# Performance work log

Hardware: AMD Instinct MI355X
Metric: run time of the kernel (lower is better)

Reference implementation:

```python
import jax, jax.numpy as jnp
import numpy as np

NUM_HEADS = 8
KEY_DIM = 512  # d_gain = 1/sqrt(key_dim) in the original (NOT per-head dim)
MASK_FILL = -1000000.0


def setup_inputs() -> dict:
    key = jax.random.key(0)
    ks = jax.random.split(key, 6)
    N, Tq, Tk, D, U = 8, 1024, 1024, 512, 512
    query = jax.random.normal(ks[0], (N, Tq, D), dtype=jnp.float32)
    key_t = jax.random.normal(ks[1], (N, Tk, D), dtype=jnp.float32)
    key_mask = jax.random.randint(ks[2], (N, Tk), 0, 2).astype(bool)
    Wq = jax.random.normal(ks[3], (D, U), dtype=jnp.float32) / np.sqrt(D)
    Wk = jax.random.normal(ks[4], (D, U), dtype=jnp.float32) / np.sqrt(D)
    Wv = jax.random.normal(ks[5], (D, U), dtype=jnp.float32) / np.sqrt(D)
    return {"query": query, "key": key_t, "key_mask": key_mask,
            "Wq": Wq, "Wk": Wk, "Wv": Wv}


def reference(query, key, key_mask, Wq, Wk, Wv):
    N, Tq, _ = query.shape
    Tk = key.shape[1]
    U = Wq.shape[1]
    h = NUM_HEADS
    d = U // h
    scale = 1.0 / (KEY_DIM ** 0.5)

    # projections then split heads: [N,T,U] -> [h,N,T,d]
    q = (query @ Wq).reshape(N, Tq, h, d).transpose(2, 0, 1, 3)
    k = (key @ Wk).reshape(N, Tk, h, d).transpose(2, 0, 1, 3)
    v = (key @ Wv).reshape(N, Tk, h, d).transpose(2, 0, 1, 3)

    scores = scale * jnp.einsum('hnqd,hnkd->hnqk', q, k)
    scores = jnp.where(key_mask[None, :, None, :], scores, MASK_FILL)
    attn = jax.nn.softmax(scores, axis=3)
    out = jnp.einsum('hnqk,hnkd->hnqd', attn, v)
    # merge heads: [h,N,Tq,d] -> [N,Tq,h*d]
    return out.transpose(1, 2, 0, 3).reshape(N, Tq, U)
```

## Files before the change

kernel.cpp:

```cpp
#include <hip/hip_runtime.h>
#include <hip/hip_bf16.h>

typedef unsigned short u16;
typedef __attribute__((ext_vector_type(8))) short short8;
typedef __attribute__((ext_vector_type(4))) short short4v;
typedef __attribute__((ext_vector_type(4))) float f32x4;

#define NB 8
#define TT 1024
#define DD 512
#define UU 512
#define HH 8
#define DH 64
#define SCALE 0.044194173824159216f
#define LOG2E 1.4426950408889634f
#define MASK_FILL_2 -1442695.0f

__device__ __forceinline__ float ld_flex(const void* p, long i, bool f32) {
  if (f32) return ((const float*)p)[i];
  unsigned int u = (unsigned int)(((const u16*)p)[i]) << 16;
  return __uint_as_float(u);
}

__device__ __forceinline__ u16 f32_to_bf16(float f) {
  unsigned int u = __float_as_uint(f);
  unsigned int r = (u + 0x7FFFu + ((u >> 16) & 1u)) >> 16;
  return (u16)r;
}

__device__ __forceinline__ float ex2(float x) {
#if __has_builtin(__builtin_amdgcn_exp2f)
  return __builtin_amdgcn_exp2f(x);
#else
  return __expf(x * 0.6931471805599453f);
#endif
}

__device__ __forceinline__ unsigned int pk_bf16(float a, float b) {
  union { __hip_bfloat162 h2; unsigned int u; } c;
  c.h2 = __float22bfloat162_rn(make_float2(a, b));
  return c.u;
}

__device__ __forceinline__ void gld16(const void* g, void* l) {
  __builtin_amdgcn_global_load_lds(
      (const __attribute__((address_space(1))) unsigned int*)g,
      (__attribute__((address_space(3))) unsigned int*)l, 16, 0, 0);
}

#define CONV_BLOCKS 2048
#define WT_BLOCKS 768
#define MASK_BLOCKS 32

__global__ __launch_bounds__(256) void prep_kernel(
    const void* __restrict__ query, const void* __restrict__ key,
    const void* __restrict__ W0, const void* __restrict__ W1,
    const void* __restrict__ W2, const void* __restrict__ mask,
    u16* __restrict__ Xq, u16* __restrict__ Xk, u16* __restrict__ Wt,
    float* __restrict__ maskadd, int* __restrict__ flags) {
  __shared__ float tile[32][33];
  __shared__ int s_f32, s_mi32;
  const int b = blockIdx.x, tid = threadIdx.x;

  if (tid == 0) { s_f32 = 0; s_mi32 = 1; }
  __syncthreads();
  {
    const u16* qh = (const u16*)query;
    int weird = 0;
#pragma unroll
    for (int p = 0; p < 4; ++p) {
      unsigned int u = (unsigned int)qh[tid * 4 + p] << 16;
      float v = __uint_as_float(u);
      if (!(v == v) || fabsf(v) > 1e6f) weird = 1;
    }
    if (weird) atomicOr(&s_f32, 1);
    const unsigned int* mi = (const unsigned int*)mask;
    if (mi[tid * 2] > 1u || mi[tid * 2 + 1] > 1u) atomicAnd(&s_mi32, 0);
  }
  __syncthreads();
  const bool f32 = s_f32 != 0;
  const bool mi32 = s_mi32 != 0;
  if (b == CONV_BLOCKS && tid == 0) { flags[0] = s_f32; flags[1] = s_mi32; }

  if (b < CONV_BLOCKS) {
    if (!f32) return;
#pragma unroll
    for (int p = 0; p < 4; ++p) {
      const int i = b * 256 + tid + p * (CONV_BLOCKS * 256);
      const void* in = (i < 1048576) ? query : key;
      u16* outp = (i < 1048576) ? Xq : Xk;
      const int j = i & 1048575;
      float4 v = ((const float4*)in)[j];
      ushort4 o;
      o.x = f32_to_bf16(v.x); o.y = f32_to_bf16(v.y);
      o.z = f32_to_bf16(v.z); o.w = f32_to_bf16(v.w);
      ((ushort4*)outp)[j] = o;
    }
  } else if (b < CONV_BLOCKS + WT_BLOCKS) {
    const int lb = b - CONV_BLOCKS;
    const int z = lb >> 8, rem = lb & 255;
    const int k0 = (rem & 15) * 32, n0 = (rem >> 4) * 32;
    const void* W = (z == 0) ? W0 : (z == 1) ? W1 : W2;
    const float sc = (z == 0) ? SCALE * LOG2E : 1.0f;
    u16* out = Wt + (size_t)z * DD * UU;
#pragma unroll
    for (int p = 0; p < 4; ++p) {
      int i = (tid >> 5) + p * 8, j = tid & 31;
      tile[i][j] = ld_flex(W, (long)(k0 + i) * UU + n0 + j, f32);
    }
    __syncthreads();
#pragma unroll
    for (int p = 0; p < 4; ++p) {
      int nl = (tid >> 5) + p * 8, kl = tid & 31;
      out[(size_t)(n0 + nl) * DD + k0 + kl] = f32_to_bf16(tile[kl][nl] * sc);
    }
  } else {
    const int i = (b - CONV_BLOCKS - WT_BLOCKS) * 256 + tid;
    bool mv = mi32 ? (((const int*)mask)[i] != 0)
                   : (((const unsigned char*)mask)[i] != 0);
    maskadd[i] = mv ? 0.0f : MASK_FILL_2;
  }
}

__global__ __launch_bounds__(256) void proj_mfma(
    const void* __restrict__ query, const void* __restrict__ key,
    const u16* __restrict__ Xq, const u16* __restrict__ Xk,
    const u16* __restrict__ Wt, u16* __restrict__ Qp, u16* __restrict__ Kp,
    u16* __restrict__ Vt, const int* __restrict__ flags) {
  __shared__ __align__(16) u16 smem[128 * 136];
  const bool f32 = flags[0] != 0;
  const int lid = blockIdx.x + (blockIdx.y << 6) + (blockIdx.z << 8);
  const int swz = (lid & 7) * 96 + (lid >> 3);
  const int bx = swz & 63, by = (swz >> 6) & 3, z = swz >> 8;
  const u16* X = (z == 0) ? (f32 ? Xq : (const u16*)query)
                          : (f32 ? Xk : (const u16*)key);
  const u16* Wz = Wt + (size_t)z * DD * UU;
  const int m0 = bx * 128, n0 = by * 128;
  const int tid = threadIdx.x;
  const int w = tid >> 6, l = tid & 63;
  const int quad = l >> 4, l15 = l & 15;
  const int wm = (w >> 1) * 64, wn = (w & 1) * 64;

  const int c0 = w * 128 + l;
  const int row0 = c0 >> 2, q0 = (c0 & 3) * 8;
  const int c1 = c0 + 64;
  const int row1 = c1 >> 2, q1 = (c1 & 3) * 8;
  const u16* aS0 = X + (size_t)(m0 + row0) * DD + q0;
  const u16* aS1 = X + (size_t)(m0 + row1) * DD + q1;
  const u16* bS0 = Wz + (size_t)(n0 + row0) * DD + q0;
  const u16* bS1 = Wz + (size_t)(n0 + row1) * DD + q1;
  const int dD0 = w * 1024;
  const int dD1 = w * 1024 + 512;

  f32x4 acc[4][4];
#pragma unroll
  for (int mi = 0; mi < 4; ++mi)
#pragma unroll
    for (int ni = 0; ni < 4; ++ni)
#pragma unroll
      for (int r = 0; r < 4; ++r) acc[mi][ni][r] = 0.0f;

  gld16(aS0, smem + dD0);
  gld16(aS1, smem + dD1);
  gld16(bS0, smem + 4096 + dD0);
  gld16(bS1, smem + 4096 + dD1);

#pragma unroll 1
  for (int t = 0; t < 16; ++t) {
    const int co = (t & 1) * 8192;
    if (t < 15) {
      const int k1 = (t + 1) * 32;
      const int no = ((t + 1) & 1) * 8192;
      gld16(aS0 + k1, smem + no + dD0);
      gld16(aS1 + k1, smem + no + dD1);
      gld16(bS0 + k1, smem + no + 4096 + dD0);
      gld16(bS1 + k1, smem + no + 4096 + dD1);
      asm volatile("s_waitcnt vmcnt(4)" ::: "memory");
    } else {
      asm volatile("s_waitcnt vmcnt(0)" ::: "memory");
    }
    __builtin_amdgcn_s_barrier();

    short8 af[4], bf[4];
#pragma unroll
    for (int mi = 0; mi < 4; ++mi)
      af[mi] = *(const short8*)&smem[co + (wm + mi * 16 + l15) * 32 + quad * 8];
#pragma unroll
    for (int ni = 0; ni < 4; ++ni)
      bf[ni] = *(const short8*)&smem[co + 4096 + (wn + ni * 16 + l15) * 32 + quad * 8];
#pragma unroll
    for (int mi = 0; mi < 4; ++mi)
#pragma unroll
      for (int ni = 0; ni < 4; ++ni)
        acc[mi][ni] = __builtin_amdgcn_mfma_f32_16x16x32_bf16(
            af[mi], bf[ni], acc[mi][ni], 0, 0, 0);
    __builtin_amdgcn_s_barrier();
  }

  if (z < 2) {
#pragma unroll
    for (int mi = 0; mi < 4; ++mi)
#pragma unroll
      for (int ni = 0; ni < 4; ++ni) {
        const int ml = wm + mi * 16 + quad * 4;
        const int nl = wn + ni * 16 + l15;
#pragma unroll
        for (int r = 0; r < 4; ++r)
          smem[(ml + r) * 136 + nl] = f32_to_bf16(acc[mi][ni][r]);
      }
  } else {
#pragma unroll
    for (int mi = 0; mi < 4; ++mi)
#pragma unroll
      for (int ni = 0; ni < 4; ++ni) {
        const int ml = wm + mi * 16 + quad * 4;
        const int nl = wn + ni * 16 + l15;
        ushort4 pk;
        pk.x = f32_to_bf16(acc[mi][ni][0]);
        pk.y = f32_to_bf16(acc[mi][ni][1]);
        pk.z = f32_to_bf16(acc[mi][ni][2]);
        pk.w = f32_to_bf16(acc[mi][ni][3]);
        *(ushort4*)&smem[nl * 136 + ml] = pk;
      }
  }
  __syncthreads();

  if (z < 2) {
    u16* outp = (z == 0) ? Qp : Kp;
#pragma unroll
    for (int p = 0; p < 8; ++p) {
      const int idx = tid + p * 256;
      const int row = idx >> 4, c8 = (idx & 15) * 8;
      short8 v = *(const short8*)&smem[row * 136 + c8];
      *(short8*)&outp[(size_t)(m0 + row) * UU + n0 + c8] = v;
    }
  } else {
    const int nb = m0 >> 10, tk0 = m0 & 1023;
#pragma unroll
    for (int p = 0; p < 8; ++p) {
      const int idx = tid + p * 256;
      const int row = idx >> 4, c8 = (idx & 15) * 8;
      const int u = n0 + row, h = u >> 6, dh = u & 63;
      short8 v = *(const short8*)&smem[row * 136 + c8];
      *(short8*)&Vt[(size_t)((nb * HH + h) * DH + dh) * TT + tk0 + c8] = v;
    }
  }
}

__global__ __launch_bounds__(256, 4) void attn_mfma(
    const u16* __restrict__ Qp, const u16* __restrict__ Kp,
    const u16* __restrict__ Vt, const float* __restrict__ maskadd,
    void* __restrict__ out, const int* __restrict__ flags) {
  __shared__ __align__(16) char smem[35072];
  u16* sU = (u16*)smem;
  const int tid = threadIdx.x;
  const int w = tid >> 6, l = tid & 63;
  const int quad = l >> 4, l15 = l & 15;
  const int lid = blockIdx.x + (blockIdx.y << 4) + (blockIdx.z << 7);
  const int swz = (lid & 7) * 128 + (lid >> 3);
  const int qt = swz & 15, h = (swz >> 4) & 7, n = swz >> 7;
  const int q0 = qt * 64;
  const bool f32o = flags[0] != 0;
  u16* s_mask = sU + 16384;
  float* lp = (float*)(smem + 34816);

  {
    float4 m4 = ((const float4*)(maskadd + n * TT))[tid];
    ushort4 mu;
    mu.x = f32_to_bf16(m4.x); mu.y = f32_to_bf16(m4.y);
    mu.z = f32_to_bf16(m4.z); mu.w = f32_to_bf16(m4.w);
    ((ushort4*)s_mask)[tid] = mu;
  }

  const u16* qbase = Qp + (size_t)(n * TT + q0 + w * 16 + l15) * UU + h * DH + quad * 8;
  short8 bq[2];
  bq[0] = *(const short8*)(qbase);
  bq[1] = *(const short8*)(qbase + 32);

  const int lr = l >> 3, ls = l & 7;
  const u16* kc = Kp + (size_t)(n * TT + w * 16 + lr) * UU + h * DH + ((ls ^ lr) * 8);
  const u16* vc = Vt + (size_t)((n * HH + h) * DH + w * 16 + lr) * TT + ((ls ^ lr) * 8);

  const int srcA = ((quad & 1) << 5) + l15;
  const int srcB = srcA + 16;
  const bool hiK = (quad >> 1) != 0;

  f32x4 o[4];
  float lsum = 0.0f;
#pragma unroll
  for (int ni = 0; ni < 4; ++ni)
#pragma unroll
    for (int r = 0; r < 4; ++r) o[ni][r] = 0.0f;

  __syncthreads();

  gld16(kc, smem + w * 2048);
  gld16(kc + 8 * UU, smem + w * 2048 + 1024);
  gld16(vc, smem + 16384 + w * 2048);
  gld16(vc + 8 * TT, smem + 16384 + w * 2048 + 1024);

#pragma unroll 1
  for (int t = 0; t < 16; ++t) {
    const int co = (t & 1) * 4096;
    if (t < 15) {
      const int no = ((t + 1) & 1) * 8192;
      const u16* kn = kc + (size_t)(t + 1) * 64 * UU;
      const u16* vn = vc + (t + 1) * 64;
      gld16(kn, smem + no + w * 2048);
      gld16(kn + 8 * UU, smem + no + w * 2048 + 1024);
      gld16(vn, smem + 16384 + no + w * 2048);
      gld16(vn + 8 * TT, smem + 16384 + no + w * 2048 + 1024);
      asm volatile("s_waitcnt vmcnt(4)" ::: "memory");
    } else {
      asm volatile("s_waitcnt vmcnt(0)" ::: "memory");
    }
    __builtin_amdgcn_s_barrier();

#pragma unroll
    for (int ss = 0; ss < 2; ++ss) {
      short8 ak[2][2];
#pragma unroll
      for (int ktl = 0; ktl < 2; ++ktl)
#pragma unroll
        for (int kd = 0; kd < 2; ++kd)
          ak[ktl][kd] = *(const short8*)&sU[co + (ss * 32 + ktl * 16 + l15) * 64 +
                                            (((kd * 4 + quad) ^ (l15 & 7)) * 8)];

      f32x4 s[2];
      __builtin_amdgcn_s_setprio(1);
#pragma unroll
      for (int ktl = 0; ktl < 2; ++ktl) {
#pragma unroll
        for (int r = 0; r < 4; ++r) s[ktl][r] = 0.0f;
#pragma unroll
        for (int kd = 0; kd < 2; ++kd)
          s[ktl] = __builtin_amdgcn_mfma_f32_16x16x32_bf16(
              ak[ktl][kd], bq[kd], s[ktl], 0, 0, 0);
      }
      __builtin_amdgcn_s_setprio(0);

      const int kb = t * 64 + ss * 32;
      unsigned int u00, u01, u10, u11;
      {
        ushort4 m0u = *(const ushort4*)&s_mask[kb + quad * 4];
        ushort4 m1u = *(const ushort4*)&s_mask[kb + 16 + quad * 4];
        float e0 = ex2(s[0][0] + __uint_as_float((unsigned)m0u.x << 16));
        float e1 = ex2(s[0][1] + __uint_as_float((unsigned)m0u.y << 16));
        float e2 = ex2(s[0][2] + __uint_as_float((unsigned)m0u.z << 16));
        float e3 = ex2(s[0][3] + __uint_as_float((unsigned)m0u.w << 16));
        float f0 = ex2(s[1][0] + __uint_as_float((unsigned)m1u.x << 16));
        float f1 = ex2(s[1][1] + __uint_as_float((unsigned)m1u.y << 16));
        float f2 = ex2(s[1][2] + __uint_as_float((unsigned)m1u.z << 16));
        float f3 = ex2(s[1][3] + __uint_as_float((unsigned)m1u.w << 16));
        lsum += ((e0 + e1) + (e2 + e3)) + ((f0 + f1) + (f2 + f3));
        u00 = pk_bf16(e0, e1); u01 = pk_bf16(e2, e3);
        u10 = pk_bf16(f0, f1); u11 = pk_bf16(f2, f3);
      }

      short8 ap;
      {
        unsigned int a0k0 = __shfl(u00, srcA), a0k1 = __shfl(u10, srcA);
        unsigned int a1k0 = __shfl(u01, srcA), a1k1 = __shfl(u11, srcA);
        unsigned int a2k0 = __shfl(u00, srcB), a2k1 = __shfl(u10, srcB);
        unsigned int a3k0 = __shfl(u01, srcB), a3k1 = __shfl(u11, srcB);
        union { unsigned int d[4]; short8 v; } pu;
        pu.d[0] = hiK ? a0k1 : a0k0;
        pu.d[1] = hiK ? a1k1 : a1k0;
        pu.d[2] = hiK ? a2k1 : a2k0;
        pu.d[3] = hiK ? a3k1 : a3k0;
        ap = pu.v;
      }

      short8 vf[4];
#pragma unroll
      for (int ni = 0; ni < 4; ++ni)
        vf[ni] = *(const short8*)&sU[8192 + co + (ni * 16 + l15) * 64 +
                                     (((ss * 4 + quad) ^ (l15 & 7)) * 8)];

      __builtin_amdgcn_s_setprio(1);
#pragma unroll
      for (int ni = 0; ni < 4; ++ni)
        o[ni] = __builtin_amdgcn_mfma_f32_16x16x32_bf16(ap, vf[ni], o[ni], 0, 0, 0);
      __builtin_amdgcn_s_setprio(0);
    }

    __builtin_amdgcn_s_barrier();
  }

  lsum += __shfl_xor(lsum, 16);
  lsum += __shfl_xor(lsum, 32);
  if (l < 16) lp[w * 16 + l] = lsum;
  __syncthreads();

  float den[4];
#pragma unroll
  for (int r = 0; r < 4; ++r) den[r] = lp[w * 16 + quad * 4 + r];

#pragma unroll
  for (int ni = 0; ni < 4; ++ni)
#pragma unroll
    for (int r = 0; r < 4; ++r) {
      const int q = q0 + w * 16 + quad * 4 + r;
      const float v = o[ni][r] / den[r];
      const size_t idx = (size_t)(n * TT + q) * UU + h * DH + ni * 16 + l15;
      if (f32o) ((float*)out)[idx] = v;
      else ((u16*)out)[idx] = f32_to_bf16(v);
    }
}

extern "C" void kernel_launch(void* const* d_in, const int* in_sizes, int n_in,
                              void* d_out, int out_size, void* d_ws, size_t ws_size,
                              hipStream_t stream) {
  const void* query = d_in[0];
  const void* key   = d_in[1];
  const void* mask  = d_in[2];
  const void* Wq    = d_in[3];
  const void* Wk    = d_in[4];
  const void* Wv    = d_in[5];

  char* base = (char*)d_ws;
  int* flags = (int*)base;
  float* maskadd = (float*)(base + 256);
  u16* Wt  = (u16*)(base + 64 * 1024);
  u16* Xq  = Wt + (size_t)3 * DD * UU;
  u16* Xk  = Xq + (size_t)NB * TT * DD;
  u16* Qp  = Xk + (size_t)NB * TT * DD;
  u16* Kp  = Qp + (size_t)NB * TT * UU;
  u16* Vtp = Kp + (size_t)NB * TT * UU;

  prep_kernel<<<CONV_BLOCKS + WT_BLOCKS + MASK_BLOCKS, 256, 0, stream>>>(
      query, key, Wq, Wk, Wv, mask, Xq, Xk, Wt, maskadd, flags);

  dim3 pgrid(NB * TT / 128, UU / 128, 3);
  proj_mfma<<<pgrid, 256, 0, stream>>>(query, key, Xq, Xk, Wt, Qp, Kp, Vtp, flags);

  dim3 agrid(TT / 64, HH, NB);
  attn_mfma<<<agrid, 256, 0, stream>>>(Qp, Kp, Vtp, maskadd, d_out, flags);
}
```

Baseline: 152.5 us.

## Split attention key range across two wave groups with shared-memory reduction

```diff
diff --git a/kernel.cpp b/kernel.cpp
--- a/kernel.cpp
+++ b/kernel.cpp
@@ -247,15 +247,16 @@
   }
 }
 
-__global__ __launch_bounds__(256, 4) void attn_mfma(
+__global__ __launch_bounds__(512, 8) void attn_mfma(
     const u16* __restrict__ Qp, const u16* __restrict__ Kp,
     const u16* __restrict__ Vt, const float* __restrict__ maskadd,
     void* __restrict__ out, const int* __restrict__ flags) {
-  __shared__ __align__(16) char smem[35072];
+  __shared__ __align__(16) char smem[35328];
   u16* sU = (u16*)smem;
   const int tid = threadIdx.x;
   const int w = tid >> 6, l = tid & 63;
   const int quad = l >> 4, l15 = l & 15;
+  const int qsub = w & 3, ks = w >> 2;
   const int lid = blockIdx.x + (blockIdx.y << 4) + (blockIdx.z << 7);
   const int swz = (lid & 7) * 128 + (lid >> 3);
   const int qt = swz & 15, h = (swz >> 4) & 7, n = swz >> 7;
@@ -264,7 +265,7 @@
   u16* s_mask = sU + 16384;
   float* lp = (float*)(smem + 34816);
 
-  {
+  if (tid < 256) {
     float4 m4 = ((const float4*)(maskadd + n * TT))[tid];
     ushort4 mu;
     mu.x = f32_to_bf16(m4.x); mu.y = f32_to_bf16(m4.y);
@@ -272,14 +273,19 @@
     ((ushort4*)s_mask)[tid] = mu;
   }
 
-  const u16* qbase = Qp + (size_t)(n * TT + q0 + w * 16 + l15) * UU + h * DH + quad * 8;
+  const u16* qbase = Qp + (size_t)(n * TT + q0 + qsub * 16 + l15) * UU + h * DH + quad * 8;
   short8 bq[2];
   bq[0] = *(const short8*)(qbase);
   bq[1] = *(const short8*)(qbase + 32);
 
-  const int lr = l >> 3, ls = l & 7;
-  const u16* kc = Kp + (size_t)(n * TT + w * 16 + lr) * UU + h * DH + ((ls ^ lr) * 8);
-  const u16* vc = Vt + (size_t)((n * HH + h) * DH + w * 16 + lr) * TT + ((ls ^ lr) * 8);
+  const int lr3 = l >> 3, ls7 = l & 7;
+  const int lr2 = l >> 2, ls3 = l & 3;
+  const u16* kc = Kp + (size_t)(n * TT + ks * 512 + qsub * 8 + lr3) * UU + h * DH +
+                  ((ls7 ^ lr3) * 8);
+  const u16* vc = Vt + (size_t)((n * HH + h) * DH + qsub * 16 + lr2) * TT + ks * 512 +
+                  ((ls3 ^ (lr2 & 3)) * 8);
+
+  const int winb = ks * 16384;
 
   const int srcA = ((quad & 1) << 5) + l15;
   const int srcB = srcA + 16;
@@ -294,95 +300,86 @@
 
   __syncthreads();
 
-  gld16(kc, smem + w * 2048);
-  gld16(kc + 8 * UU, smem + w * 2048 + 1024);
-  gld16(vc, smem + 16384 + w * 2048);
-  gld16(vc + 8 * TT, smem + 16384 + w * 2048 + 1024);
+  gld16(kc, smem + winb + qsub * 1024);
+  gld16(vc, smem + winb + 8192 + qsub * 1024);
 
 #pragma unroll 1
   for (int t = 0; t < 16; ++t) {
-    const int co = (t & 1) * 4096;
+    const int cu = (winb >> 1) + (t & 1) * 2048;
     if (t < 15) {
-      const int no = ((t + 1) & 1) * 8192;
-      const u16* kn = kc + (size_t)(t + 1) * 64 * UU;
-      const u16* vn = vc + (t + 1) * 64;
-      gld16(kn, smem + no + w * 2048);
-      gld16(kn + 8 * UU, smem + no + w * 2048 + 1024);
-      gld16(vn, smem + 16384 + no + w * 2048);
-      gld16(vn + 8 * TT, smem + 16384 + no + w * 2048 + 1024);
-      asm volatile("s_waitcnt vmcnt(4)" ::: "memory");
+      const int nob = winb + ((t + 1) & 1) * 4096;
+      gld16(kc + (size_t)(t + 1) * 32 * UU, smem + nob + qsub * 1024);
+      gld16(vc + (t + 1) * 32, smem + nob + 8192 + qsub * 1024);
+      asm volatile("s_waitcnt vmcnt(2)" ::: "memory");
     } else {
       asm volatile("s_waitcnt vmcnt(0)" ::: "memory");
     }
     __builtin_amdgcn_s_barrier();
 
-#pragma unroll
-    for (int ss = 0; ss < 2; ++ss) {
-      short8 ak[2][2];
-#pragma unroll
-      for (int ktl = 0; ktl < 2; ++ktl)
-#pragma unroll
-        for (int kd = 0; kd < 2; ++kd)
-          ak[ktl][kd] = *(const short8*)&sU[co + (ss * 32 + ktl * 16 + l15) * 64 +
-                                            (((kd * 4 + quad) ^ (l15 & 7)) * 8)];
-
-      f32x4 s[2];
-      __builtin_amdgcn_s_setprio(1);
-#pragma unroll
-      for (int ktl = 0; ktl < 2; ++ktl) {
-#pragma unroll
-        for (int r = 0; r < 4; ++r) s[ktl][r] = 0.0f;
-#pragma unroll
-        for (int kd = 0; kd < 2; ++kd)
-          s[ktl] = __builtin_amdgcn_mfma_f32_16x16x32_bf16(
-              ak[ktl][kd], bq[kd], s[ktl], 0, 0, 0);
-      }
-      __builtin_amdgcn_s_setprio(0);
-
-      const int kb = t * 64 + ss * 32;
-      unsigned int u00, u01, u10, u11;
-      {
-        ushort4 m0u = *(const ushort4*)&s_mask[kb + quad * 4];
-        ushort4 m1u = *(const ushort4*)&s_mask[kb + 16 + quad * 4];
-        float e0 = ex2(s[0][0] + __uint_as_float((unsigned)m0u.x << 16));
-        float e1 = ex2(s[0][1] + __uint_as_float((unsigned)m0u.y << 16));
-        float e2 = ex2(s[0][2] + __uint_as_float((unsigned)m0u.z << 16));
-        float e3 = ex2(s[0][3] + __uint_as_float((unsigned)m0u.w << 16));
-        float f0 = ex2(s[1][0] + __uint_as_float((unsigned)m1u.x << 16));
-        float f1 = ex2(s[1][1] + __uint_as_float((unsigned)m1u.y << 16));
-        float f2 = ex2(s[1][2] + __uint_as_float((unsigned)m1u.z << 16));
-        float f3 = ex2(s[1][3] + __uint_as_float((unsigned)m1u.w << 16));
-        lsum += ((e0 + e1) + (e2 + e3)) + ((f0 + f1) + (f2 + f3));
-        u00 = pk_bf16(e0, e1); u01 = pk_bf16(e2, e3);
-        u10 = pk_bf16(f0, f1); u11 = pk_bf16(f2, f3);
-      }
-
-      short8 ap;
-      {
-        unsigned int a0k0 = __shfl(u00, srcA), a0k1 = __shfl(u10, srcA);
-        unsigned int a1k0 = __shfl(u01, srcA), a1k1 = __shfl(u11, srcA);
-        unsigned int a2k0 = __shfl(u00, srcB), a2k1 = __shfl(u10, srcB);
-        unsigned int a3k0 = __shfl(u01, srcB), a3k1 = __shfl(u11, srcB);
-        union { unsigned int d[4]; short8 v; } pu;
-        pu.d[0] = hiK ? a0k1 : a0k0;
-        pu.d[1] = hiK ? a1k1 : a1k0;
-        pu.d[2] = hiK ? a2k1 : a2k0;
-        pu.d[3] = hiK ? a3k1 : a3k0;
-        ap = pu.v;
-      }
-
-      short8 vf[4];
-#pragma unroll
-      for (int ni = 0; ni < 4; ++ni)
-        vf[ni] = *(const short8*)&sU[8192 + co + (ni * 16 + l15) * 64 +
-                                     (((ss * 4 + quad) ^ (l15 & 7)) * 8)];
-
-      __builtin_amdgcn_s_setprio(1);
-#pragma unroll
-      for (int ni = 0; ni < 4; ++ni)
-        o[ni] = __builtin_amdgcn_mfma_f32_16x16x32_bf16(ap, vf[ni], o[ni], 0, 0, 0);
-      __builtin_amdgcn_s_setprio(0);
-    }
+    const int kb = ks * 512 + t * 32;
+    short8 ak[2][2];
+#pragma unroll
+    for (int ktl = 0; ktl < 2; ++ktl)
+#pragma unroll
+      for (int kd = 0; kd < 2; ++kd)
+        ak[ktl][kd] = *(const short8*)&sU[cu + (ktl * 16 + l15) * 64 +
+                                          (((kd * 4 + quad) ^ (l15 & 7)) * 8)];
+
+    f32x4 s[2];
+    __builtin_amdgcn_s_setprio(1);
+#pragma unroll
+    for (int ktl = 0; ktl < 2; ++ktl) {
+#pragma unroll
+      for (int r = 0; r < 4; ++r) s[ktl][r] = 0.0f;
+#pragma unroll
+      for (int kd = 0; kd < 2; ++kd)
+        s[ktl] = __builtin_amdgcn_mfma_f32_16x16x32_bf16(
+            ak[ktl][kd], bq[kd], s[ktl], 0, 0, 0);
+    }
+    __builtin_amdgcn_s_setprio(0);
+
+    unsigned int u00, u01, u10, u11;
+    {
+      ushort4 m0u = *(const ushort4*)&s_mask[kb + quad * 4];
+      ushort4 m1u = *(const ushort4*)&s_mask[kb + 16 + quad * 4];
+      float e0 = ex2(s[0][0] + __uint_as_float((unsigned)m0u.x << 16));
+      float e1 = ex2(s[0][1] + __uint_as_float((unsigned)m0u.y << 16));
+      float e2 = ex2(s[0][2] + __uint_as_float((unsigned)m0u.z << 16));
+      float e3 = ex2(s[0][3] + __uint_as_float((unsigned)m0u.w << 16));
+      float f0 = ex2(s[1][0] + __uint_as_float((unsigned)m1u.x << 16));
+      float f1 = ex2(s[1][1] + __uint_as_float((unsigned)m1u.y << 16));
+      float f2 = ex2(s[1][2] + __uint_as_float((unsigned)m1u.z << 16));
+      float f3 = ex2(s[1][3] + __uint_as_float((unsigned)m1u.w << 16));
+      lsum += ((e0 + e1) + (e2 + e3)) + ((f0 + f1) + (f2 + f3));
+      u00 = pk_bf16(e0, e1); u01 = pk_bf16(e2, e3);
+      u10 = pk_bf16(f0, f1); u11 = pk_bf16(f2, f3);
+    }
+
+    short8 ap;
+    {
+      unsigned int a0k0 = __shfl(u00, srcA), a0k1 = __shfl(u10, srcA);
+      unsigned int a1k0 = __shfl(u01, srcA), a1k1 = __shfl(u11, srcA);
+      unsigned int a2k0 = __shfl(u00, srcB), a2k1 = __shfl(u10, srcB);
+      unsigned int a3k0 = __shfl(u01, srcB), a3k1 = __shfl(u11, srcB);
+      union { unsigned int d[4]; short8 v; } pu;
+      pu.d[0] = hiK ? a0k1 : a0k0;
+      pu.d[1] = hiK ? a1k1 : a1k0;
+      pu.d[2] = hiK ? a2k1 : a2k0;
+      pu.d[3] = hiK ? a3k1 : a3k0;
+      ap = pu.v;
+    }
+
+    short8 vf[4];
+#pragma unroll
+    for (int ni = 0; ni < 4; ++ni)
+      vf[ni] = *(const short8*)&sU[cu + 4096 + (ni * 16 + l15) * 32 +
+                                   ((quad ^ (l15 & 3)) * 8)];
+
+    __builtin_amdgcn_s_setprio(1);
+#pragma unroll
+    for (int ni = 0; ni < 4; ++ni)
+      o[ni] = __builtin_amdgcn_mfma_f32_16x16x32_bf16(ap, vf[ni], o[ni], 0, 0, 0);
+    __builtin_amdgcn_s_setprio(0);
 
     __builtin_amdgcn_s_barrier();
   }
@@ -390,22 +387,35 @@
   lsum += __shfl_xor(lsum, 16);
   lsum += __shfl_xor(lsum, 32);
   if (l < 16) lp[w * 16 + l] = lsum;
-  __syncthreads();
-
-  float den[4];
-#pragma unroll
-  for (int r = 0; r < 4; ++r) den[r] = lp[w * 16 + quad * 4 + r];
-
-#pragma unroll
-  for (int ni = 0; ni < 4; ++ni)
-#pragma unroll
-    for (int r = 0; r < 4; ++r) {
-      const int q = q0 + w * 16 + quad * 4 + r;
-      const float v = o[ni][r] / den[r];
-      const size_t idx = (size_t)(n * TT + q) * UU + h * DH + ni * 16 + l15;
-      if (f32o) ((float*)out)[idx] = v;
-      else ((u16*)out)[idx] = f32_to_bf16(v);
-    }
+
+  __syncthreads();
+  if (ks == 1) {
+    float* Ost = (float*)smem + qsub * 1024;
+#pragma unroll
+    for (int ni = 0; ni < 4; ++ni)
+#pragma unroll
+      for (int r = 0; r < 4; ++r)
+        Ost[(quad * 4 + r) * 64 + ni * 16 + l15] = o[ni][r];
+  }
+  __syncthreads();
+
+  if (ks == 0) {
+    float* Ost = (float*)smem + qsub * 1024;
+    float den[4];
+#pragma unroll
+    for (int r = 0; r < 4; ++r)
+      den[r] = lp[w * 16 + quad * 4 + r] + lp[(w + 4) * 16 + quad * 4 + r];
+#pragma unroll
+    for (int ni = 0; ni < 4; ++ni)
+#pragma unroll
+      for (int r = 0; r < 4; ++r) {
+        const int q = q0 + qsub * 16 + quad * 4 + r;
+        const float v = (o[ni][r] + Ost[(quad * 4 + r) * 64 + ni * 16 + l15]) / den[r];
+        const size_t idx = (size_t)(n * TT + q) * UU + h * DH + ni * 16 + l15;
+        if (f32o) ((float*)out)[idx] = v;
+        else ((u16*)out)[idx] = f32_to_bf16(v);
+      }
+  }
 }
 
 extern "C" void kernel_launch(void* const* d_in, const int* in_sizes, int n_in,
@@ -435,5 +445,5 @@
   proj_mfma<<<pgrid, 256, 0, stream>>>(query, key, Xq, Xk, Wt, Qp, Kp, Vtp, flags);
 
   dim3 agrid(TT / 64, HH, NB);
-  attn_mfma<<<agrid, 256, 0, stream>>>(Qp, Kp, Vtp, maskadd, d_out, flags);
-}
+  attn_mfma<<<agrid, 512, 0, stream>>>(Qp, Kp, Vtp, maskadd, d_out, flags);
+}
```

Result: no change. 154.2 us (+1.1%).
